# Kernel optimization log

Hardware: AMD Instinct MI355X
Metric: run time of the kernel (lower is better)

The kernel has to match this reference:

```python
import jax, jax.numpy as jnp
import numpy as np

B, P, S, FX, FY, D, DFF = 8, 1, 2048, 16, 16, 512, 2048


def _ln(x, g, b, eps=1e-6):
    m = jnp.mean(x, axis=-1, keepdims=True)
    v = jnp.var(x, axis=-1, keepdims=True)
    return g * (x - m) / jnp.sqrt(v + eps) + b


def setup_inputs() -> dict:
    key = jax.random.key(0)
    ks = jax.random.split(key, 16)
    sc = 0.02
    inp = {
        'inputs': jax.random.normal(ks[0], (B, P, S, FX), dtype=jnp.float32),
        'targets': jax.random.normal(ks[1], (B, P, S, FY), dtype=jnp.float32),
        # input projection Dense(d_model)
        'Wp': jax.random.normal(ks[2], (FX, D), dtype=jnp.float32) * sc,
        'bp': jnp.zeros((D,), jnp.float32),
        # attention projections wq/wk/wv/dense (all Dense(d_model))
        'Wq': jax.random.normal(ks[3], (D, D), dtype=jnp.float32) * sc,
        'bq': jnp.zeros((D,), jnp.float32),
        'Wk': jax.random.normal(ks[4], (D, D), dtype=jnp.float32) * sc,
        'bk': jnp.zeros((D,), jnp.float32),
        'Wv': jax.random.normal(ks[5], (D, D), dtype=jnp.float32) * sc,
        'bv': jnp.zeros((D,), jnp.float32),
        'Wo': jax.random.normal(ks[6], (D, D), dtype=jnp.float32) * sc,
        'bo': jnp.zeros((D,), jnp.float32),
        # layernorm 1 / 2
        'g1': jnp.ones((D,), jnp.float32),
        'beta1': jnp.zeros((D,), jnp.float32),
        'g2': jnp.ones((D,), jnp.float32),
        'beta2': jnp.zeros((D,), jnp.float32),
        # pointwise FFN Dense(dff, relu) -> Dense(d_model)
        'Wf1': jax.random.normal(ks[7], (D, DFF), dtype=jnp.float32) * sc,
        'bf1': jnp.zeros((DFF,), jnp.float32),
        'Wf2': jax.random.normal(ks[8], (DFF, D), dtype=jnp.float32) * sc,
        'bf2': jnp.zeros((D,), jnp.float32),
        # final output layer Dense(output_size)
        'Wfin': jax.random.normal(ks[9], (D, FY), dtype=jnp.float32) * sc,
        'bfin': jnp.zeros((FY,), jnp.float32),
    }
    return inp


def reference(inputs, targets, Wp, bp, Wq, bq, Wk, bk, Wv, bv, Wo, bo,
              g1, beta1, g2, beta2, Wf1, bf1, Wf2, bf2, Wfin, bfin):
    d = jnp.float32(Wp.shape[1])
    # projection_layer_ts then *sqrt(d_model)
    x = (inputs @ Wp + bp) * jnp.sqrt(d)                      # (B,P,S,D)
    q = x @ Wq + bq
    k = x @ Wk + bk
    v = x @ Wv + bv
    # with noise=False and no resampling, the per-step SMC recurrence equals
    # causal self-attention (at step t, K/V hold rows <= t, rest are zero-masked)
    logits = jnp.einsum('bpqd,bpkd->bpqk', q, k) / jnp.sqrt(d)  # (B,P,S,S)
    Sdim = x.shape[2]
    causal = jnp.tril(jnp.ones((Sdim, Sdim), dtype=bool))
    logits = jnp.where(causal, logits, jnp.float32(-1e9))
    attn = jax.nn.softmax(logits, axis=-1)                    # attention weights per step
    z = jnp.einsum('bpqk,bpkd->bpqd', attn, v)
    z = z @ Wo + bo
    # full_model: LN(z+x) -> FFN -> LN(ffn+out)
    out = _ln(z + x, g1, beta1)
    ff = jax.nn.relu(out @ Wf1 + bf1) @ Wf2 + bf2
    r = _ln(ff + out, g2, beta2)                              # R trajectory (B,P,S,D)
    pred = r @ Wfin + bfin                                    # (B,P,S,F_y)
    # no resampling (noise=False): R_resampl == R, pred_resampl == pred
    return (pred, pred, k, v, r, attn)
```

## Files before the change

### kernel.cpp

```cpp
#include <hip/hip_runtime.h>
#include <hip/hip_bf16.h>
#include <stdint.h>

#define BB 8
#define SS 2048
#define TT (BB*SS)
#define DD 512
#define DFFX 2048

static __device__ const float SQRTD  = 22.627416997969522f;
static __device__ const float INVSQD = 0.04419417382415922f;

typedef __attribute__((ext_vector_type(4))) float  f32x4_t;
typedef __attribute__((ext_vector_type(8))) __bf16 bf16x8_t;
typedef __attribute__((ext_vector_type(4))) __bf16 bf16x4_t;
typedef __attribute__((ext_vector_type(2))) __bf16 bf16x2_t;

static __device__ __forceinline__ bf16x8_t mk_frag(bf16x4_t lo, bf16x4_t hi) {
  return __builtin_shufflevector(lo, hi, 0, 1, 2, 3, 4, 5, 6, 7);
}

typedef __attribute__((address_space(1))) const unsigned int g_u32;
typedef __attribute__((address_space(3))) unsigned int lds_u32;
static __device__ __forceinline__ void gld16(const void* g, void* l) {
  __builtin_amdgcn_global_load_lds((g_u32*)g, (lds_u32*)l, 16, 0, 0);
}

__global__ __launch_bounds__(256) void transpose_conv3(
    const float* __restrict__ Wo, const float* __restrict__ Wf1,
    const float* __restrict__ Wf2, __bf16* __restrict__ Wo_t,
    __bf16* __restrict__ Wf1_t, __bf16* __restrict__ Wf2_t) {
  const int bx = blockIdx.x;
  const float* src; __bf16* dst; int C, R, gx, gy;
  if (bx < 256)       { src = Wo;  dst = Wo_t;  R = 512;  C = 512;  gx = bx & 15;  gy = bx >> 4; }
  else if (bx < 1280) { const int b = bx - 256;  src = Wf1; dst = Wf1_t; R = 512;  C = 2048; gx = b & 63; gy = b >> 6; }
  else                { const int b = bx - 1280; src = Wf2; dst = Wf2_t; R = 2048; C = 512;  gx = b & 15; gy = b >> 4; }
  __shared__ float tile[32][33];
  const int c0 = gx * 32, r0 = gy * 32;
  const int tx = threadIdx.x & 31, ty = threadIdx.x >> 5;
#pragma unroll
  for (int i = 0; i < 4; i++)
    tile[ty + 8*i][tx] = src[(size_t)(r0 + ty + 8*i) * C + c0 + tx];
  __syncthreads();
#pragma unroll
  for (int i = 0; i < 4; i++)
    dst[(size_t)(c0 + ty + 8*i) * R + r0 + tx] = (__bf16)tile[tx][ty + 8*i];
}

__global__ __launch_bounds__(256) void fold_kernel(
    const float* __restrict__ Wp, const float* __restrict__ bp,
    const float* __restrict__ Wq, const float* __restrict__ bq,
    const float* __restrict__ Wk, const float* __restrict__ bk,
    const float* __restrict__ Wv, const float* __restrict__ bv,
    float* __restrict__ Wfold, float* __restrict__ bfold) {
  __shared__ float wp[16][512];
  __shared__ float bps[512];
  for (int i = threadIdx.x; i < 16 * 512; i += 256) wp[i >> 9][i & 511] = Wp[i];
  for (int i = threadIdx.x; i < 512; i += 256) bps[i] = bp[i];
  __syncthreads();
  const int cl = threadIdx.x & 15, r = threadIdx.x >> 4;
  const int cg = blockIdx.x * 16 + cl;
  const int sub = cg >> 9, wc = cg & 511;
  const float* W = sub == 0 ? Wq : sub == 1 ? Wk : Wv;
  const float* bb = sub == 0 ? bq : sub == 1 ? bk : bv;
  float acc = 0.f, bacc = 0.f;
  for (int k = 0; k < 512; k += 4) {
    const float4 wpv = *(const float4*)&wp[r][k];
    const float g0 = W[(size_t)k * 512 + wc];
    const float g1 = W[(size_t)(k + 1) * 512 + wc];
    const float g2 = W[(size_t)(k + 2) * 512 + wc];
    const float g3 = W[(size_t)(k + 3) * 512 + wc];
    acc += wpv.x * g0 + wpv.y * g1 + wpv.z * g2 + wpv.w * g3;
    if (r == 0) {
      const float4 b4 = *(const float4*)&bps[k];
      bacc += b4.x * g0 + b4.y * g1 + b4.z * g2 + b4.w * g3;
    }
  }
  Wfold[(size_t)r * 1536 + cg] = acc * SQRTD;
  if (r == 0) bfold[cg] = bacc * SQRTD + bb[wc];
}

__global__ __launch_bounds__(256) void smallk_kernel(
    const float* __restrict__ inp,
    const float* __restrict__ Wfold, const float* __restrict__ bfold,
    const float* __restrict__ Wp, const float* __restrict__ bp,
    __bf16* __restrict__ qb, __bf16* __restrict__ kb, __bf16* __restrict__ vb,
    __bf16* __restrict__ xb, float* __restrict__ o_k, float* __restrict__ o_v) {
  const int sl = blockIdx.y;
  const float* W; const float* bias; int ldw; float scale;
  __bf16* ob; float* fo;
  if (sl == 3) { W = Wp; bias = bp; ldw = 512; scale = SQRTD; ob = xb; fo = nullptr; }
  else {
    W = Wfold + sl * 512; bias = bfold + sl * 512; ldw = 1536; scale = 1.f;
    ob = sl == 0 ? qb : sl == 1 ? kb : vb;
    fo = sl == 0 ? (float*)nullptr : sl == 1 ? o_k : o_v;
  }
  __shared__ float ivl[16][16];
  const int tid = threadIdx.x;
  ivl[tid >> 4][tid & 15] = inp[(size_t)blockIdx.x * 256 + tid];
  const int c0 = 2 * tid;
  float w0[16], w1[16];
#pragma unroll
  for (int r = 0; r < 16; r++) {
    w0[r] = W[(size_t)r * ldw + c0];
    w1[r] = W[(size_t)r * ldw + c0 + 1];
  }
  const float bb0 = bias[c0], bb1 = bias[c0 + 1];
  __syncthreads();
#pragma unroll 4
  for (int tt = 0; tt < 16; ++tt) {
    const float4 i0 = *(const float4*)&ivl[tt][0];
    const float4 i1 = *(const float4*)&ivl[tt][4];
    const float4 i2 = *(const float4*)&ivl[tt][8];
    const float4 i3 = *(const float4*)&ivl[tt][12];
    float a0, a1;
    a0  = i0.x * w0[0];   a1  = i0.x * w1[0];
    a0 += i0.y * w0[1];   a1 += i0.y * w1[1];
    a0 += i0.z * w0[2];   a1 += i0.z * w1[2];
    a0 += i0.w * w0[3];   a1 += i0.w * w1[3];
    a0 += i1.x * w0[4];   a1 += i1.x * w1[4];
    a0 += i1.y * w0[5];   a1 += i1.y * w1[5];
    a0 += i1.z * w0[6];   a1 += i1.z * w1[6];
    a0 += i1.w * w0[7];   a1 += i1.w * w1[7];
    a0 += i2.x * w0[8];   a1 += i2.x * w1[8];
    a0 += i2.y * w0[9];   a1 += i2.y * w1[9];
    a0 += i2.z * w0[10];  a1 += i2.z * w1[10];
    a0 += i2.w * w0[11];  a1 += i2.w * w1[11];
    a0 += i3.x * w0[12];  a1 += i3.x * w1[12];
    a0 += i3.y * w0[13];  a1 += i3.y * w1[13];
    a0 += i3.z * w0[14];  a1 += i3.z * w1[14];
    a0 += i3.w * w0[15];  a1 += i3.w * w1[15];
    const float v0 = (a0 + bb0) * scale;
    const float v1 = (a1 + bb1) * scale;
    const size_t t = (size_t)blockIdx.x * 16 + tt;
    bf16x2_t pv; pv[0] = (__bf16)v0; pv[1] = (__bf16)v1;
    *(bf16x2_t*)(ob + t * 512 + c0) = pv;
    if (fo) {
      float2 fv; fv.x = v0; fv.y = v1;
      *(float2*)(fo + t * 512 + c0) = fv;
    }
  }
}

template <bool CTRI, bool CAUSAL, bool RELU, bool RES, bool SCALE, bool CT, bool PAIR>
__global__ __launch_bounds__(256) void gemm128(
    const __bf16* __restrict__ A, const __bf16* __restrict__ Bt,
    const float* __restrict__ bias, const __bf16* __restrict__ Res,
    __bf16* __restrict__ Cb, float* __restrict__ Cf,
    int N, int K, size_t aBatch, size_t bBatch, size_t cBatch) {
  const int n0 = blockIdx.x * 128;
  if (CTRI && !PAIR && n0 > (int)blockIdx.y * 128 + 127) return;
  __shared__ __align__(16) __bf16 As[3 * 128 * 32];
  __shared__ __align__(16) __bf16 Bs[3 * 128 * 32];
  const int tid = threadIdx.x, lane = tid & 63, wave = tid >> 6;
  const int l15 = lane & 15, g = lane >> 4;
  const int wr = wave >> 1, wc = wave & 1;

  const int srow0 = wave * 32 + (lane >> 2);
  const int srow1 = srow0 + 16;
  const int sc0 = (((lane & 3) ^ ((srow0 >> 1) & 3)) << 4);
  const int sc1 = (((lane & 3) ^ ((srow1 >> 1) & 3)) << 4);
  const size_t aOff = (size_t)blockIdx.z * aBatch;
  const size_t bOff = (size_t)blockIdx.z * bBatch;
  const size_t cOff = (size_t)blockIdx.z * cBatch;
  const char* gb0 = (const char*)(Bt + bOff + (size_t)(n0 + srow0) * K) + sc0;
  const char* gb1 = (const char*)(Bt + bOff + (size_t)(n0 + srow1) * K) + sc1;

  const int plo = (g >> 1) ^ ((l15 >> 1) & 3);
  const int aof0 = (wr * 64 + l15) * 64 + plo * 16 + (g & 1) * 8;
  const int bof0 = (wc * 64 + l15) * 64 + plo * 16 + (g & 1) * 8;

  const int nhalf = PAIR ? 2 : 1;
#pragma unroll
  for (int half = 0; half < nhalf; ++half) {
    const int mb = (half == 0) ? (int)blockIdx.y
                               : (2 * (int)gridDim.y - 1 - (int)blockIdx.y);
    const int m0 = mb * 128;
    const char* ga0 = (const char*)(A + aOff + (size_t)(m0 + srow0) * K) + sc0;
    const char* ga1 = (const char*)(A + aOff + (size_t)(m0 + srow1) * K) + sc1;

    f32x4_t acc[4][4];
#pragma unroll
    for (int i = 0; i < 4; i++)
#pragma unroll
      for (int j = 0; j < 4; j++) acc[i][j] = (f32x4_t){0.f, 0.f, 0.f, 0.f};

    auto STAGE = [&](const int buf, const int k0) {
      const size_t kb = (size_t)k0 * 2;
      char* la = (char*)As + buf * 8192 + wave * 2048;
      char* lb = (char*)Bs + buf * 8192 + wave * 2048;
      gld16(ga0 + kb, la);
      gld16(ga1 + kb, la + 1024);
      gld16(gb0 + kb, lb);
      gld16(gb1 + kb, lb + 1024);
    };
    auto COMPUTE = [&](const int buf) {
      const char* AsB = (const char*)As + buf * 8192;
      const char* BsB = (const char*)Bs + buf * 8192;
      bf16x8_t af[4], bfr[4];
#pragma unroll
      for (int i = 0; i < 4; i++) {
        const int ao = aof0 + i * 1024;
        af[i] = mk_frag(*(const bf16x4_t*)(AsB + ao),
                        *(const bf16x4_t*)(AsB + (ao ^ 32)));
        const int bo = bof0 + i * 1024;
        bfr[i] = mk_frag(*(const bf16x4_t*)(BsB + bo),
                         *(const bf16x4_t*)(BsB + (bo ^ 32)));
      }
#pragma unroll
      for (int i = 0; i < 4; i++)
#pragma unroll
        for (int j = 0; j < 4; j++)
          acc[i][j] = __builtin_amdgcn_mfma_f32_16x16x32_bf16(af[i], bfr[j], acc[i][j], 0, 0, 0);
    };

    const int kend = CAUSAL ? (m0 + 128) : K;
    const int nt = kend >> 5;
    STAGE(0, 0);
    STAGE(1, 32);
    STAGE(2, 64);
    int cur = 0;
    for (int t = 0; t < nt; ++t) {
      const int rem = nt - 1 - t;
      if (rem >= 2)      asm volatile("s_waitcnt vmcnt(8)" ::: "memory");
      else if (rem == 1) asm volatile("s_waitcnt vmcnt(4)" ::: "memory");
      else               asm volatile("s_waitcnt vmcnt(0)" ::: "memory");
      __builtin_amdgcn_s_barrier();
      COMPUTE(cur);
      __builtin_amdgcn_s_barrier();
      if (t + 3 < nt) STAGE(cur, (t + 3) << 5);
      cur = (cur == 2) ? 0 : cur + 1;
    }

#pragma unroll
    for (int i = 0; i < 4; i++) {
#pragma unroll
      for (int j = 0; j < 4; j++) {
        const int col = n0 + wc * 64 + j * 16 + l15;
        if (CT) {
          const int row0 = m0 + wr * 64 + i * 16 + g * 4;
          bf16x4_t tv;
#pragma unroll
          for (int r = 0; r < 4; r++) tv[r] = (__bf16)acc[i][j][r];
          *(bf16x4_t*)(Cb + cOff + (size_t)col * SS + row0) = tv;
        } else {
          const float bv = bias ? bias[col] : 0.f;
#pragma unroll
          for (int r = 0; r < 4; r++) {
            const int row = m0 + wr * 64 + i * 16 + g * 4 + r;
            float v = acc[i][j][r];
            if (SCALE) v *= INVSQD;
            v += bv;
            if (RELU) v = fmaxf(v, 0.f);
            if (RES) v += (float)Res[cOff + (size_t)row * N + col];
            const size_t cidx = cOff + (size_t)row * N + col;
            if (Cb) Cb[cidx] = (__bf16)v;
            if (Cf) Cf[cidx] = v;
          }
        }
      }
    }
  }
}

__global__ __launch_bounds__(256) void softmax_kernel(
    float* __restrict__ att, __bf16* __restrict__ pb) {
  const int t = blockIdx.x * 4 + (threadIdx.x >> 6);
  const int gq = t & (SS - 1);
  const int lane = threadIdx.x & 63;
  float* row = att + (size_t)t * SS;
  __bf16* prow = pb + (size_t)t * SS;
  const int nch = (gq >> 9) + 1;
  const int wlim = ((gq & ~127) + 128 + 511) >> 9;
  float x[32];
  float m = -1e30f;
#pragma unroll
  for (int ch = 0; ch < 4; ch++) {
    float* xp = &x[ch * 8];
    if (ch < nch) {
      const int c0 = ch * 512 + lane * 8;
      bf16x8_t v = *(const bf16x8_t*)(prow + c0);
#pragma unroll
      for (int j = 0; j < 8; j++) {
        const float f = (float)v[j];
        xp[j] = (c0 + j <= gq) ? f : -1e30f;
        m = fmaxf(m, xp[j]);
      }
    } else {
#pragma unroll
      for (int j = 0; j < 8; j++) xp[j] = -1e30f;
    }
  }
#pragma unroll
  for (int off = 1; off < 64; off <<= 1) m = fmaxf(m, __shfl_xor(m, off, 64));
  float s = 0.f;
#pragma unroll
  for (int i = 0; i < 32; i++) { x[i] = __expf(x[i] - m); s += x[i]; }
#pragma unroll
  for (int off = 1; off < 64; off <<= 1) s += __shfl_xor(s, off, 64);
  const float inv = 1.f / s;
#pragma unroll
  for (int ch = 0; ch < 4; ch++) {
    const int c0 = ch * 512 + lane * 8;
    float o[8];
    bf16x8_t ov;
#pragma unroll
    for (int j = 0; j < 8; j++) {
      const float pv = x[ch * 8 + j] * inv;
      o[j] = pv;
      ov[j] = (__bf16)pv;
    }
    float4 f0, f1;
    f0.x = o[0]; f0.y = o[1]; f0.z = o[2]; f0.w = o[3];
    f1.x = o[4]; f1.y = o[5]; f1.z = o[6]; f1.w = o[7];
    *(float4*)(row + c0) = f0;
    *(float4*)(row + c0 + 4) = f1;
    if (ch < wlim) *(bf16x8_t*)(prow + c0) = ov;
  }
}

__global__ __launch_bounds__(256) void ln_kernel(
    const __bf16* __restrict__ X, const float* __restrict__ gam,
    const float* __restrict__ bet, __bf16* __restrict__ Ob, float* __restrict__ Of) {
  const int t = blockIdx.x * 4 + (threadIdx.x >> 6);
  const int lane = threadIdx.x & 63;
  const int d0 = lane * 8;
  bf16x8_t xv = *(const bf16x8_t*)(X + (size_t)t * DD + d0);
  float x[8];
#pragma unroll
  for (int j = 0; j < 8; j++) x[j] = (float)xv[j];
  float s = 0.f, sq = 0.f;
#pragma unroll
  for (int j = 0; j < 8; j++) { s += x[j]; sq += x[j] * x[j]; }
#pragma unroll
  for (int off = 1; off < 64; off <<= 1) {
    s += __shfl_xor(s, off, 64);
    sq += __shfl_xor(sq, off, 64);
  }
  const float mean = s * (1.f / 512.f);
  const float var = sq * (1.f / 512.f) - mean * mean;
  const float rstd = rsqrtf(var + 1e-6f);
  float4 g0 = *(const float4*)(gam + d0), g1v = *(const float4*)(gam + d0 + 4);
  float4 b0 = *(const float4*)(bet + d0), b1v = *(const float4*)(bet + d0 + 4);
  float gg[8] = {g0.x, g0.y, g0.z, g0.w, g1v.x, g1v.y, g1v.z, g1v.w};
  float bb2[8] = {b0.x, b0.y, b0.z, b0.w, b1v.x, b1v.y, b1v.z, b1v.w};
  float o[8];
#pragma unroll
  for (int j = 0; j < 8; j++) o[j] = (x[j] - mean) * rstd * gg[j] + bb2[j];
  if (Ob) {
    bf16x8_t ov;
#pragma unroll
    for (int j = 0; j < 8; j++) ov[j] = (__bf16)o[j];
    *(bf16x8_t*)(Ob + (size_t)t * DD + d0) = ov;
  }
  if (Of) {
    float4 f0; f0.x = o[0]; f0.y = o[1]; f0.z = o[2]; f0.w = o[3];
    float4 f1; f1.x = o[4]; f1.y = o[5]; f1.z = o[6]; f1.w = o[7];
    *(float4*)(Of + (size_t)t * DD + d0) = f0;
    *(float4*)(Of + (size_t)t * DD + d0 + 4) = f1;
  }
}

__global__ __launch_bounds__(256) void final_kernel(
    const float* __restrict__ Rm, const float* __restrict__ Wfin,
    const float* __restrict__ bfin, float* __restrict__ P1, float* __restrict__ P2) {
  __shared__ float wfs[512][17];
  for (int i = threadIdx.x; i < 512 * 16; i += 256) wfs[i >> 4][i & 15] = Wfin[i];
  __syncthreads();
  const int tl = threadIdx.x >> 4, n = threadIdx.x & 15;
  const int t = blockIdx.x * 16 + tl;
  const float* rp = Rm + (size_t)t * DD;
  float acc = 0.f;
#pragma unroll 4
  for (int k = 0; k < 512; k += 4) {
    float4 rv = *(const float4*)(rp + k);
    acc += rv.x * wfs[k][n] + rv.y * wfs[k + 1][n] + rv.z * wfs[k + 2][n] + rv.w * wfs[k + 3][n];
  }
  const float v = acc + bfin[n];
  P1[(size_t)t * 16 + n] = v;
  P2[(size_t)t * 16 + n] = v;
}

extern "C" void kernel_launch(void* const* d_in, const int* in_sizes, int n_in,
                              void* d_out, int out_size, void* d_ws, size_t ws_size,
                              hipStream_t stream) {
  const float* inp  = (const float*)d_in[0];
  const float* Wp   = (const float*)d_in[2];
  const float* bp   = (const float*)d_in[3];
  const float* Wq   = (const float*)d_in[4];
  const float* bq   = (const float*)d_in[5];
  const float* Wk   = (const float*)d_in[6];
  const float* bk   = (const float*)d_in[7];
  const float* Wv   = (const float*)d_in[8];
  const float* bv   = (const float*)d_in[9];
  const float* Wo   = (const float*)d_in[10];
  const float* bo   = (const float*)d_in[11];
  const float* g1   = (const float*)d_in[12];
  const float* be1  = (const float*)d_in[13];
  const float* g2   = (const float*)d_in[14];
  const float* be2  = (const float*)d_in[15];
  const float* Wf1  = (const float*)d_in[16];
  const float* bf1  = (const float*)d_in[17];
  const float* Wf2  = (const float*)d_in[18];
  const float* bf2  = (const float*)d_in[19];
  const float* Wfin = (const float*)d_in[20];
  const float* bfin = (const float*)d_in[21];
  (void)in_sizes; (void)n_in; (void)out_size; (void)ws_size;

  float* out = (float*)d_out;
  float* o_pred1 = out;
  float* o_pred2 = out + 262144;
  float* o_k     = out + 524288;
  float* o_v     = out + 8912896;
  float* o_r     = out + 17301504;
  float* o_att   = out + 25690112;

  char* base = (char*)d_ws;
  size_t off = 0;
  auto takeB = [&](size_t bytes) -> char* {
    char* p = base + off;
    off += (bytes + 255) & ~(size_t)255;
    return p;
  };
  float*  Wfold = (float*)takeB((size_t)16 * 1536 * 4);
  float*  bfold = (float*)takeB((size_t)1536 * 4);
  __bf16* Wo_t  = (__bf16*)takeB((size_t)DD * DD * 2);
  __bf16* Wf1_t = (__bf16*)takeB((size_t)DD * DFFX * 2);
  __bf16* Wf2_t = (__bf16*)takeB((size_t)DD * DFFX * 2);
  __bf16* xb    = (__bf16*)takeB((size_t)TT * DD * 2);
  __bf16* qbuf  = (__bf16*)takeB((size_t)TT * DD * 2);
  __bf16* kbuf  = (__bf16*)takeB((size_t)TT * DD * 2);
  __bf16* vbuf  = (__bf16*)takeB((size_t)TT * DD * 2);
  __bf16* vwt   = (__bf16*)takeB((size_t)TT * DD * 2);
  __bf16* h1b   = (__bf16*)takeB((size_t)TT * DD * 2);
  __bf16* lninb = (__bf16*)takeB((size_t)TT * DD * 2);
  __bf16* ffb   = (__bf16*)takeB((size_t)TT * DFFX * 2);
  __bf16* pb    = ffb;

  transpose_conv3<<<dim3(2304), 256, 0, stream>>>(Wo, Wf1, Wf2, Wo_t, Wf1_t, Wf2_t);

  fold_kernel<<<dim3(96), 256, 0, stream>>>(Wp, bp, Wq, bq, Wk, bk, Wv, bv,
                                            Wfold, bfold);

  smallk_kernel<<<dim3(TT / 16, 4), 256, 0, stream>>>(
      inp, Wfold, bfold, Wp, bp, qbuf, kbuf, vbuf, xb, o_k, o_v);

  gemm128<true, false, false, false, true, false, false><<<dim3(16, 16, BB), 256, 0, stream>>>(
      qbuf, kbuf, nullptr, nullptr, pb, nullptr, SS, DD,
      (size_t)SS * DD, (size_t)SS * DD, (size_t)SS * SS);

  gemm128<false, false, false, false, false, true, false><<<dim3(4, 16, BB), 256, 0, stream>>>(
      vbuf, Wo_t, nullptr, nullptr, vwt, nullptr, DD, DD,
      (size_t)SS * DD, 0, (size_t)SS * DD);

  softmax_kernel<<<dim3(TT / 4), 256, 0, stream>>>(o_att, pb);

  gemm128<false, true, false, true, false, false, true><<<dim3(4, 8, BB), 256, 0, stream>>>(
      pb, vwt, bo, xb, lninb, nullptr, DD, SS,
      (size_t)SS * SS, (size_t)DD * SS, (size_t)SS * DD);

  ln_kernel<<<dim3(TT / 4), 256, 0, stream>>>(lninb, g1, be1, h1b, nullptr);

  gemm128<false, false, true, false, false, false, false><<<dim3(16, 128, 1), 256, 0, stream>>>(
      h1b, Wf1_t, bf1, nullptr, ffb, nullptr, DFFX, DD, 0, 0, 0);
  gemm128<false, false, false, true, false, false, false><<<dim3(4, 128, 1), 256, 0, stream>>>(
      ffb, Wf2_t, bf2, h1b, lninb, nullptr, DD, DFFX, 0, 0, 0);

  ln_kernel<<<dim3(TT / 4), 256, 0, stream>>>(lninb, g2, be2, nullptr, o_r);
  final_kernel<<<dim3(TT / 16), 256, 0, stream>>>(o_r, Wfin, bfin, o_pred1, o_pred2);
}
```

Baseline: 472.2 us.

## Add wide 128x256 GEMM tiles and fuse final LayerNorm with output projection

Adds a WIDE template variant to the bf16 MFMA GEMM that computes a 128x256 output tile per block, reusing A fragments across two column halves. It is used for the V·Wo and both FFN GEMMs to cut A-operand reloads. The final LayerNorm and prediction projection are merged into one kernel, avoiding a global round-trip of R. The trade-offs are doubled accumulator registers, which may reduce occupancy, and Wfin being staged into LDS for every 4-token block.

Result: slower. 568.2 us (+20.3%).

```diff
diff --git a/kernel.cpp b/kernel.cpp
--- a/kernel.cpp
+++ b/kernel.cpp
@@ -142,29 +142,33 @@
   }
 }
 
-template <bool CTRI, bool CAUSAL, bool RELU, bool RES, bool SCALE, bool CT, bool PAIR>
+template <bool CTRI, bool CAUSAL, bool RELU, bool RES, bool SCALE, bool CT,
+          bool PAIR, bool WIDE>
 __global__ __launch_bounds__(256) void gemm128(
     const __bf16* __restrict__ A, const __bf16* __restrict__ Bt,
     const float* __restrict__ bias, const __bf16* __restrict__ Res,
     __bf16* __restrict__ Cb, float* __restrict__ Cf,
     int N, int K, size_t aBatch, size_t bBatch, size_t cBatch) {
-  const int n0 = blockIdx.x * 128;
+  constexpr int NH  = WIDE ? 2 : 1;
+  constexpr int NBQ = WIDE ? 4 : 2;
+  constexpr int BSTRIDE = WIDE ? 16384 : 8192;
+  const int n0 = blockIdx.x * (WIDE ? 256 : 128);
   if (CTRI && !PAIR && n0 > (int)blockIdx.y * 128 + 127) return;
   __shared__ __align__(16) __bf16 As[3 * 128 * 32];
-  __shared__ __align__(16) __bf16 Bs[3 * 128 * 32];
+  __shared__ __align__(16) __bf16 Bs[WIDE ? 3 * 256 * 32 : 3 * 128 * 32];
   const int tid = threadIdx.x, lane = tid & 63, wave = tid >> 6;
   const int l15 = lane & 15, g = lane >> 4;
   const int wr = wave >> 1, wc = wave & 1;
 
-  const int srow0 = wave * 32 + (lane >> 2);
-  const int srow1 = srow0 + 16;
-  const int sc0 = (((lane & 3) ^ ((srow0 >> 1) & 3)) << 4);
-  const int sc1 = (((lane & 3) ^ ((srow1 >> 1) & 3)) << 4);
+  const int sc = (((lane & 3) ^ ((lane >> 3) & 3)) << 4);
   const size_t aOff = (size_t)blockIdx.z * aBatch;
   const size_t bOff = (size_t)blockIdx.z * bBatch;
   const size_t cOff = (size_t)blockIdx.z * cBatch;
-  const char* gb0 = (const char*)(Bt + bOff + (size_t)(n0 + srow0) * K) + sc0;
-  const char* gb1 = (const char*)(Bt + bOff + (size_t)(n0 + srow1) * K) + sc1;
+  const char* gb[NBQ];
+#pragma unroll
+  for (int q = 0; q < NBQ; q++)
+    gb[q] = (const char*)(Bt + bOff +
+            (size_t)(n0 + wave * (WIDE ? 64 : 32) + q * 16 + (lane >> 2)) * K) + sc;
 
   const int plo = (g >> 1) ^ ((l15 >> 1) & 3);
   const int aof0 = (wr * 64 + l15) * 64 + plo * 16 + (g & 1) * 8;
@@ -176,42 +180,53 @@
     const int mb = (half == 0) ? (int)blockIdx.y
                                : (2 * (int)gridDim.y - 1 - (int)blockIdx.y);
     const int m0 = mb * 128;
-    const char* ga0 = (const char*)(A + aOff + (size_t)(m0 + srow0) * K) + sc0;
-    const char* ga1 = (const char*)(A + aOff + (size_t)(m0 + srow1) * K) + sc1;
-
-    f32x4_t acc[4][4];
+    const char* ga0 = (const char*)(A + aOff +
+        (size_t)(m0 + wave * 32 + (lane >> 2)) * K) + sc;
+    const char* ga1 = ga0 + (size_t)16 * K * 2;
+
+    f32x4_t acc[4][4][NH];
 #pragma unroll
     for (int i = 0; i < 4; i++)
 #pragma unroll
-      for (int j = 0; j < 4; j++) acc[i][j] = (f32x4_t){0.f, 0.f, 0.f, 0.f};
+      for (int j = 0; j < 4; j++)
+#pragma unroll
+        for (int h = 0; h < NH; h++) acc[i][j][h] = (f32x4_t){0.f, 0.f, 0.f, 0.f};
 
     auto STAGE = [&](const int buf, const int k0) {
       const size_t kb = (size_t)k0 * 2;
       char* la = (char*)As + buf * 8192 + wave * 2048;
-      char* lb = (char*)Bs + buf * 8192 + wave * 2048;
       gld16(ga0 + kb, la);
       gld16(ga1 + kb, la + 1024);
-      gld16(gb0 + kb, lb);
-      gld16(gb1 + kb, lb + 1024);
+      char* lb = (char*)Bs + buf * BSTRIDE + wave * (WIDE ? 4096 : 2048);
+#pragma unroll
+      for (int q = 0; q < NBQ; q++) gld16(gb[q] + kb, lb + q * 1024);
     };
     auto COMPUTE = [&](const int buf) {
       const char* AsB = (const char*)As + buf * 8192;
-      const char* BsB = (const char*)Bs + buf * 8192;
-      bf16x8_t af[4], bfr[4];
+      const char* BsB = (const char*)Bs + buf * BSTRIDE;
+      bf16x8_t af[4], bfr[4][NH];
 #pragma unroll
       for (int i = 0; i < 4; i++) {
         const int ao = aof0 + i * 1024;
         af[i] = mk_frag(*(const bf16x4_t*)(AsB + ao),
                         *(const bf16x4_t*)(AsB + (ao ^ 32)));
-        const int bo = bof0 + i * 1024;
-        bfr[i] = mk_frag(*(const bf16x4_t*)(BsB + bo),
-                         *(const bf16x4_t*)(BsB + (bo ^ 32)));
       }
 #pragma unroll
-      for (int i = 0; i < 4; i++)
-#pragma unroll
-        for (int j = 0; j < 4; j++)
-          acc[i][j] = __builtin_amdgcn_mfma_f32_16x16x32_bf16(af[i], bfr[j], acc[i][j], 0, 0, 0);
+      for (int h = 0; h < NH; h++)
+#pragma unroll
+        for (int j = 0; j < 4; j++) {
+          const int bo = bof0 + j * 1024 + h * 8192;
+          bfr[j][h] = mk_frag(*(const bf16x4_t*)(BsB + bo),
+                              *(const bf16x4_t*)(BsB + (bo ^ 32)));
+        }
+#pragma unroll
+      for (int h = 0; h < NH; h++)
+#pragma unroll
+        for (int i = 0; i < 4; i++)
+#pragma unroll
+          for (int j = 0; j < 4; j++)
+            acc[i][j][h] = __builtin_amdgcn_mfma_f32_16x16x32_bf16(
+                af[i], bfr[j][h], acc[i][j][h], 0, 0, 0);
     };
 
     const int kend = CAUSAL ? (m0 + 128) : K;
@@ -222,9 +237,15 @@
     int cur = 0;
     for (int t = 0; t < nt; ++t) {
       const int rem = nt - 1 - t;
-      if (rem >= 2)      asm volatile("s_waitcnt vmcnt(8)" ::: "memory");
-      else if (rem == 1) asm volatile("s_waitcnt vmcnt(4)" ::: "memory");
-      else               asm volatile("s_waitcnt vmcnt(0)" ::: "memory");
+      if (WIDE) {
+        if (rem >= 2)      asm volatile("s_waitcnt vmcnt(12)" ::: "memory");
+        else if (rem == 1) asm volatile("s_waitcnt vmcnt(6)" ::: "memory");
+        else               asm volatile("s_waitcnt vmcnt(0)" ::: "memory");
+      } else {
+        if (rem >= 2)      asm volatile("s_waitcnt vmcnt(8)" ::: "memory");
+        else if (rem == 1) asm volatile("s_waitcnt vmcnt(4)" ::: "memory");
+        else               asm volatile("s_waitcnt vmcnt(0)" ::: "memory");
+      }
       __builtin_amdgcn_s_barrier();
       COMPUTE(cur);
       __builtin_amdgcn_s_barrier();
@@ -233,29 +254,32 @@
     }
 
 #pragma unroll
-    for (int i = 0; i < 4; i++) {
-#pragma unroll
-      for (int j = 0; j < 4; j++) {
-        const int col = n0 + wc * 64 + j * 16 + l15;
-        if (CT) {
-          const int row0 = m0 + wr * 64 + i * 16 + g * 4;
-          bf16x4_t tv;
-#pragma unroll
-          for (int r = 0; r < 4; r++) tv[r] = (__bf16)acc[i][j][r];
-          *(bf16x4_t*)(Cb + cOff + (size_t)col * SS + row0) = tv;
-        } else {
-          const float bv = bias ? bias[col] : 0.f;
-#pragma unroll
-          for (int r = 0; r < 4; r++) {
-            const int row = m0 + wr * 64 + i * 16 + g * 4 + r;
-            float v = acc[i][j][r];
-            if (SCALE) v *= INVSQD;
-            v += bv;
-            if (RELU) v = fmaxf(v, 0.f);
-            if (RES) v += (float)Res[cOff + (size_t)row * N + col];
-            const size_t cidx = cOff + (size_t)row * N + col;
-            if (Cb) Cb[cidx] = (__bf16)v;
-            if (Cf) Cf[cidx] = v;
+    for (int h = 0; h < NH; h++) {
+#pragma unroll
+      for (int i = 0; i < 4; i++) {
+#pragma unroll
+        for (int j = 0; j < 4; j++) {
+          const int col = n0 + h * 128 + wc * 64 + j * 16 + l15;
+          if (CT) {
+            const int row0 = m0 + wr * 64 + i * 16 + g * 4;
+            bf16x4_t tv;
+#pragma unroll
+            for (int r = 0; r < 4; r++) tv[r] = (__bf16)acc[i][j][h][r];
+            *(bf16x4_t*)(Cb + cOff + (size_t)col * SS + row0) = tv;
+          } else {
+            const float bv = bias ? bias[col] : 0.f;
+#pragma unroll
+            for (int r = 0; r < 4; r++) {
+              const int row = m0 + wr * 64 + i * 16 + g * 4 + r;
+              float v = acc[i][j][h][r];
+              if (SCALE) v *= INVSQD;
+              v += bv;
+              if (RELU) v = fmaxf(v, 0.f);
+              if (RES) v += (float)Res[cOff + (size_t)row * N + col];
+              const size_t cidx = cOff + (size_t)row * N + col;
+              if (Cb) Cb[cidx] = (__bf16)v;
+              if (Cf) Cf[cidx] = v;
+            }
           }
         }
       }
@@ -361,24 +385,63 @@
   }
 }
 
-__global__ __launch_bounds__(256) void final_kernel(
-    const float* __restrict__ Rm, const float* __restrict__ Wfin,
-    const float* __restrict__ bfin, float* __restrict__ P1, float* __restrict__ P2) {
-  __shared__ float wfs[512][17];
+__global__ __launch_bounds__(256) void ln_final_kernel(
+    const __bf16* __restrict__ X, const float* __restrict__ gam,
+    const float* __restrict__ bet, float* __restrict__ Of,
+    const float* __restrict__ Wfin, const float* __restrict__ bfin,
+    float* __restrict__ P1, float* __restrict__ P2) {
+  __shared__ float wfs[512][16];
+  __shared__ float rf[4][516];
   for (int i = threadIdx.x; i < 512 * 16; i += 256) wfs[i >> 4][i & 15] = Wfin[i];
+  const int tw = threadIdx.x >> 6;
+  const int t = blockIdx.x * 4 + tw;
+  const int lane = threadIdx.x & 63;
+  const int d0 = lane * 8;
+  bf16x8_t xv = *(const bf16x8_t*)(X + (size_t)t * DD + d0);
+  float x[8];
+#pragma unroll
+  for (int j = 0; j < 8; j++) x[j] = (float)xv[j];
+  float s = 0.f, sq = 0.f;
+#pragma unroll
+  for (int j = 0; j < 8; j++) { s += x[j]; sq += x[j] * x[j]; }
+#pragma unroll
+  for (int off = 1; off < 64; off <<= 1) {
+    s += __shfl_xor(s, off, 64);
+    sq += __shfl_xor(sq, off, 64);
+  }
+  const float mean = s * (1.f / 512.f);
+  const float var = sq * (1.f / 512.f) - mean * mean;
+  const float rstd = rsqrtf(var + 1e-6f);
+  float4 g0 = *(const float4*)(gam + d0), g1v = *(const float4*)(gam + d0 + 4);
+  float4 b0 = *(const float4*)(bet + d0), b1v = *(const float4*)(bet + d0 + 4);
+  float gg[8] = {g0.x, g0.y, g0.z, g0.w, g1v.x, g1v.y, g1v.z, g1v.w};
+  float bb2[8] = {b0.x, b0.y, b0.z, b0.w, b1v.x, b1v.y, b1v.z, b1v.w};
+  float o[8];
+  float4 f0, f1;
+#pragma unroll
+  for (int j = 0; j < 8; j++) {
+    o[j] = (x[j] - mean) * rstd * gg[j] + bb2[j];
+    rf[tw][d0 + j] = o[j];
+  }
+  f0.x = o[0]; f0.y = o[1]; f0.z = o[2]; f0.w = o[3];
+  f1.x = o[4]; f1.y = o[5]; f1.z = o[6]; f1.w = o[7];
+  *(float4*)(Of + (size_t)t * DD + d0) = f0;
+  *(float4*)(Of + (size_t)t * DD + d0 + 4) = f1;
   __syncthreads();
-  const int tl = threadIdx.x >> 4, n = threadIdx.x & 15;
-  const int t = blockIdx.x * 16 + tl;
-  const float* rp = Rm + (size_t)t * DD;
-  float acc = 0.f;
+  if (threadIdx.x < 64) {
+    const int tt = threadIdx.x >> 4, n = threadIdx.x & 15;
+    float acc = 0.f;
 #pragma unroll 4
-  for (int k = 0; k < 512; k += 4) {
-    float4 rv = *(const float4*)(rp + k);
-    acc += rv.x * wfs[k][n] + rv.y * wfs[k + 1][n] + rv.z * wfs[k + 2][n] + rv.w * wfs[k + 3][n];
-  }
-  const float v = acc + bfin[n];
-  P1[(size_t)t * 16 + n] = v;
-  P2[(size_t)t * 16 + n] = v;
+    for (int k = 0; k < 512; k += 4) {
+      const float4 rv = *(const float4*)&rf[tt][k];
+      acc += rv.x * wfs[k][n] + rv.y * wfs[k + 1][n] +
+             rv.z * wfs[k + 2][n] + rv.w * wfs[k + 3][n];
+    }
+    const float v = acc + bfin[n];
+    const size_t tok = (size_t)blockIdx.x * 4 + tt;
+    P1[tok * 16 + n] = v;
+    P2[tok * 16 + n] = v;
+  }
 }
 
 extern "C" void kernel_launch(void* const* d_in, const int* in_sizes, int n_in,
@@ -445,27 +508,32 @@
   smallk_kernel<<<dim3(TT / 16, 4), 256, 0, stream>>>(
       inp, Wfold, bfold, Wp, bp, qbuf, kbuf, vbuf, xb, o_k, o_v);
 
-  gemm128<true, false, false, false, true, false, false><<<dim3(16, 16, BB), 256, 0, stream>>>(
+  gemm128<true, false, false, false, true, false, false, false>
+      <<<dim3(16, 16, BB), 256, 0, stream>>>(
       qbuf, kbuf, nullptr, nullptr, pb, nullptr, SS, DD,
       (size_t)SS * DD, (size_t)SS * DD, (size_t)SS * SS);
 
-  gemm128<false, false, false, false, false, true, false><<<dim3(4, 16, BB), 256, 0, stream>>>(
+  gemm128<false, false, false, false, false, true, false, true>
+      <<<dim3(2, 16, BB), 256, 0, stream>>>(
       vbuf, Wo_t, nullptr, nullptr, vwt, nullptr, DD, DD,
       (size_t)SS * DD, 0, (size_t)SS * DD);
 
   softmax_kernel<<<dim3(TT / 4), 256, 0, stream>>>(o_att, pb);
 
-  gemm128<false, true, false, true, false, false, true><<<dim3(4, 8, BB), 256, 0, stream>>>(
+  gemm128<false, true, false, true, false, false, true, false>
+      <<<dim3(4, 8, BB), 256, 0, stream>>>(
       pb, vwt, bo, xb, lninb, nullptr, DD, SS,
       (size_t)SS * SS, (size_t)DD * SS, (size_t)SS * DD);
 
   ln_kernel<<<dim3(TT / 4), 256, 0, stream>>>(lninb, g1, be1, h1b, nullptr);
 
-  gemm128<false, false, true, false, false, false, false><<<dim3(16, 128, 1), 256, 0, stream>>>(
+  gemm128<false, false, true, false, false, false, false, true>
+      <<<dim3(8, 128, 1), 256, 0, stream>>>(
       h1b, Wf1_t, bf1, nullptr, ffb, nullptr, DFFX, DD, 0, 0, 0);
-  gemm128<false, false, false, true, false, false, false><<<dim3(4, 128, 1), 256, 0, stream>>>(
+  gemm128<false, false, false, true, false, false, false, true>
+      <<<dim3(2, 128, 1), 256, 0, stream>>>(
       ffb, Wf2_t, bf2, h1b, lninb, nullptr, DD, DFFX, 0, 0, 0);
 
-  ln_kernel<<<dim3(TT / 4), 256, 0, stream>>>(lninb, g2, be2, nullptr, o_r);
-  final_kernel<<<dim3(TT / 16), 256, 0, stream>>>(o_r, Wfin, bfin, o_pred1, o_pred2);
-}
+  ln_final_kernel<<<dim3(TT / 4), 256, 0, stream>>>(
+      lninb, g2, be2, o_r, Wfin, bfin, o_pred1, o_pred2);
+}
```
